# Kernel tuning notes

Hardware: AMD Instinct MI355X
Metric: run time of the kernel (lower is better)

Reference implementation:

```python
import jax, jax.numpy as jnp
import numpy as np

HEADS = 16
D_K = 64
D_MODEL = HEADS * D_K  # 1024
QUERY_DIM = 1024
B, N = 4, 2048


def setup_inputs() -> dict:
    key = jax.random.key(0)
    k1, k2, k3, k4 = jax.random.split(key, 4)
    x = jax.random.normal(k1, (B, N, QUERY_DIM), dtype=jnp.float32)
    # weights stored as [in, out]; torch Linear(in,out,bias=False) is x @ W.T with W [out,in] -- math-equivalent for random init
    Wq = jax.random.normal(k2, (QUERY_DIM, D_MODEL), dtype=jnp.float32) * (QUERY_DIM ** -0.5)
    Wkv = jax.random.normal(k3, (QUERY_DIM, 2 * D_MODEL), dtype=jnp.float32) * (QUERY_DIM ** -0.5)
    Wo = jax.random.normal(k4, (D_MODEL, QUERY_DIM), dtype=jnp.float32) * (D_MODEL ** -0.5)
    return {"x": x, "Wq": Wq, "Wkv": Wkv, "Wo": Wo}


def reference(x, Wq, Wkv, Wo):
    # self-attention: context = x
    scale = D_K ** -0.5
    q = x @ Wq                      # [b, n, h*d]
    kv = x @ Wkv                    # [b, n, 2*h*d]
    k, v = jnp.split(kv, 2, axis=-1)
    # 'b n (h d) -> b h n d'
    def split_heads(t):
        b, n, _ = t.shape
        return t.reshape(b, n, HEADS, D_K).transpose(0, 2, 1, 3)
    q, k, v = map(split_heads, (q, k, v))
    scores = jnp.einsum('bhnd,bhmd->bhnm', q, k) * scale
    attn = jax.nn.softmax(scores, axis=-1)
    out = jnp.einsum('bhnm,bhmd->bhnd', attn, v)
    out = out.transpose(0, 2, 1, 3).reshape(x.shape[0], x.shape[1], D_MODEL)
    return out @ Wo  # dropout is identity at eval
```

## Files before the change

### kernel.cpp

```cpp
#include <hip/hip_runtime.h>
#include <stdint.h>


#define NSEQ   2048
#define BQ     4
#define NTOK   (BQ * NSEQ)
#define DMODEL 1024
#define DK     64
#define HEADS  16

using bf16x8 = __attribute__((ext_vector_type(8))) short;
using u16x8  = __attribute__((ext_vector_type(8))) unsigned short;
using u16x4  = __attribute__((ext_vector_type(4))) unsigned short;
using f32x4  = __attribute__((ext_vector_type(4))) float;

#define AS1C(p) ((const __attribute__((address_space(1))) void*)(p))
#define AS3(p)  ((__attribute__((address_space(3))) void*)(p))

__device__ __forceinline__ unsigned short f2bf(float f) {
    unsigned int u = __float_as_uint(f);
    u += 0x7FFFu + ((u >> 16) & 1u);
    return (unsigned short)(u >> 16);
}


__global__ __launch_bounds__(256) void cvt_x_kernel(const float4* __restrict__ in,
                                                    u16x4* __restrict__ out) {
    int idx = blockIdx.x * 256 + threadIdx.x;
    float4 v = in[idx];
    u16x4 o;
    o[0] = f2bf(v.x); o[1] = f2bf(v.y); o[2] = f2bf(v.z); o[3] = f2bf(v.w);
    out[idx] = o;
}

__global__ __launch_bounds__(256) void transpose_cvt_kernel(const float* __restrict__ in,
                                                            unsigned short* __restrict__ out,
                                                            int K, int Nn) {
    __shared__ float t[32][33];
    int c0 = blockIdx.x * 32;
    int r0 = blockIdx.y * 32;
    int tx = threadIdx.x;
    int ty = threadIdx.y;
#pragma unroll
    for (int i = 0; i < 4; i++) {
        int r = ty + i * 8;
        t[r][tx] = in[(size_t)(r0 + r) * Nn + c0 + tx];
    }
    __syncthreads();
#pragma unroll
    for (int i = 0; i < 4; i++) {
        int r = ty + i * 8;
        out[(size_t)(c0 + r) * K + r0 + tx] = f2bf(t[tx][r]);
    }
}

template <int MODE>
__global__ __launch_bounds__(256) void gemm_bf16_kernel(
    const unsigned short* __restrict__ A,
    const unsigned short* __restrict__ BT,
    unsigned short* __restrict__ C0,
    unsigned short* __restrict__ C1,
    float* __restrict__ CF,
    int M, int N, int K) {
    __shared__ __align__(16) char smem[32768];
    char* As = smem;
    char* Bs = smem + 16384;

    const int tid  = threadIdx.x;
    const int wid  = tid >> 6;
    const int lane = tid & 63;
    const int g    = lane >> 4;
    const int lr   = lane & 15;
    const int wr   = wid >> 1;
    const int wc   = wid & 1;
    const int row0 = blockIdx.y * 128;
    const int col0 = blockIdx.x * 128;

    f32x4 acc[4][4];
#pragma unroll
    for (int i = 0; i < 4; i++)
#pragma unroll
        for (int j = 0; j < 4; j++) acc[i][j] = f32x4{0.f, 0.f, 0.f, 0.f};

    for (int kt = 0; kt < K; kt += 64) {
#pragma unroll
        for (int c = 0; c < 4; c++) {
            int ch  = c * 4 + wid;
            int off = ch * 1024 + lane * 16;
            int row = off >> 7;
            int ss  = ((off >> 4) & 7) ^ (row & 7);
            __builtin_amdgcn_global_load_lds(
                AS1C(A + (size_t)(row0 + row) * K + kt + ss * 8),
                AS3(As + ch * 1024), 16, 0, 0);
        }
#pragma unroll
        for (int c = 0; c < 4; c++) {
            int ch  = c * 4 + wid;
            int off = ch * 1024 + lane * 16;
            int row = off >> 7;
            int ss  = ((off >> 4) & 7) ^ (row & 7);
            __builtin_amdgcn_global_load_lds(
                AS1C(BT + (size_t)(col0 + row) * K + kt + ss * 8),
                AS3(Bs + ch * 1024), 16, 0, 0);
        }
        __syncthreads();

#pragma unroll
        for (int kk = 0; kk < 2; kk++) {
            bf16x8 af[4], bfr[4];
#pragma unroll
            for (int mf = 0; mf < 4; mf++) {
                int row = wr * 64 + mf * 16 + lr;
                int sl  = (kk * 4 + g) ^ (row & 7);
                af[mf]  = *(const bf16x8*)(As + row * 128 + sl * 16);
            }
#pragma unroll
            for (int nf = 0; nf < 4; nf++) {
                int row = wc * 64 + nf * 16 + lr;
                int sl  = (kk * 4 + g) ^ (row & 7);
                bfr[nf] = *(const bf16x8*)(Bs + row * 128 + sl * 16);
            }
#pragma unroll
            for (int mf = 0; mf < 4; mf++)
#pragma unroll
                for (int nf = 0; nf < 4; nf++)
                    acc[mf][nf] = __builtin_amdgcn_mfma_f32_16x16x32_bf16(
                        af[mf], bfr[nf], acc[mf][nf], 0, 0, 0);
        }
        __syncthreads();
    }

    const float SCALE = 0.125f * 1.44269504088896340736f;
#pragma unroll
    for (int mf = 0; mf < 4; mf++)
#pragma unroll
        for (int nf = 0; nf < 4; nf++) {
            if (MODE == 1 && col0 >= 1024) {
                int jj = col0 - 1024 + wc * 64 + nf * 16 + lr;
                int h  = jj >> 6, d = jj & 63;
                int n0 = row0 + wr * 64 + mf * 16 + g * 4;
                int b  = n0 >> 11, nn = n0 & 2047;
                u16x4 pk;
#pragma unroll
                for (int r = 0; r < 4; r++) pk[r] = f2bf(acc[mf][nf][r]);
                *(u16x4*)(C1 + (((size_t)(b * 16 + h)) * 64 + d) * 2048 + nn) = pk;
            } else {
#pragma unroll
                for (int r = 0; r < 4; r++) {
                    int grow = row0 + wr * 64 + mf * 16 + g * 4 + r;
                    int gcol = col0 + wc * 64 + nf * 16 + lr;
                    float v  = acc[mf][nf][r];
                    if (MODE == 2) {
                        CF[(size_t)grow * N + gcol] = v;
                    } else if (MODE == 0) {
                        int b = grow >> 11, n = grow & 2047;
                        int h = gcol >> 6, d = gcol & 63;
                        C0[(((size_t)(b * 16 + h)) * 2048 + n) * 64 + d] = f2bf(v * SCALE);
                    } else {
                        int b = grow >> 11, n = grow & 2047;
                        int h = gcol >> 6, d = gcol & 63;
                        C0[(((size_t)(b * 16 + h)) * 2048 + n) * 64 + d] = f2bf(v);
                    }
                }
            }
        }
}

__global__ __launch_bounds__(256) void attn_fwd_kernel(
    const unsigned short* __restrict__ Q,
    const unsigned short* __restrict__ K,
    const unsigned short* __restrict__ Vt,
    unsigned short* __restrict__ O) {
    __shared__ __align__(16) char smem[32768];

    const int tid  = threadIdx.x;
    const int wid  = tid >> 6;
    const int lane = tid & 63;
    const int g    = lane >> 4;
    const int lr   = lane & 15;
    const int bh   = blockIdx.y;
    const int b    = bh >> 4;
    const int h    = bh & 15;
    const size_t hb = (size_t)bh * NSEQ * DK;
    const unsigned short* Qh  = Q + hb;
    const unsigned short* Kh  = K + hb;
    const unsigned short* Vth = Vt + hb;
    const int qw = blockIdx.x * 64 + wid * 16;

    const int srow  = lane >> 3;
    const int sslot = (lane & 7) ^ srow;
    const int kOff0 = (wid * 8 + srow) * 64 + sslot * 8;
    const int kOff1 = ((wid + 4) * 8 + srow) * 64 + sslot * 8;
    const int vOff0 = (wid * 8 + srow) * 2048 + sslot * 8;
    const int vOff1 = ((wid + 4) * 8 + srow) * 2048 + sslot * 8;

    int kByte[2][4];
#pragma unroll
    for (int kk = 0; kk < 2; kk++)
#pragma unroll
        for (int kb = 0; kb < 4; kb++) {
            int row = (lr >> 2) * 8 + 2 * (lr & 3) + (kb & 1) * 32 + (kb >> 1);
            int sl  = (kk * 4 + g) ^ (row & 7);
            kByte[kk][kb] = row * 128 + sl * 16;
        }
    int vByte[2][4];
#pragma unroll
    for (int kc = 0; kc < 2; kc++)
#pragma unroll
        for (int db = 0; db < 4; db++) {
            int d = db * 16 + lr;
            int sl = (kc * 4 + g) ^ (d & 7);
            vByte[kc][db] = d * 128 + sl * 16;
        }

    bf16x8 qf[2];
#pragma unroll
    for (int kk = 0; kk < 2; kk++)
        qf[kk] = *(const bf16x8*)(Qh + (size_t)(qw + lr) * 64 + kk * 32 + g * 8);

    float l = 0.f;
    f32x4 acc_o[4];
#pragma unroll
    for (int d = 0; d < 4; d++) acc_o[d] = f32x4{0.f, 0.f, 0.f, 0.f};

    auto STAGE = [&](int buf, int kv0) {
        char* Kb = smem + buf * 8192;
        char* Vb = smem + 16384 + buf * 8192;
        __builtin_amdgcn_global_load_lds(AS1C(Kh + (size_t)kv0 * 64 + kOff0),
                                         AS3(Kb + wid * 1024), 16, 0, 0);
        __builtin_amdgcn_global_load_lds(AS1C(Kh + (size_t)kv0 * 64 + kOff1),
                                         AS3(Kb + (wid + 4) * 1024), 16, 0, 0);
        __builtin_amdgcn_global_load_lds(AS1C(Vth + kv0 + vOff0),
                                         AS3(Vb + wid * 1024), 16, 0, 0);
        __builtin_amdgcn_global_load_lds(AS1C(Vth + kv0 + vOff1),
                                         AS3(Vb + (wid + 4) * 1024), 16, 0, 0);
    };

    STAGE(0, 0);
    int cur = 0;

    for (int kvt = 0; kvt < NSEQ / 64; kvt++) {
        __syncthreads();
        if (kvt + 1 < NSEQ / 64) STAGE(cur ^ 1, (kvt + 1) * 64);

        char* Kb = smem + cur * 8192;
        char* Vb = smem + 16384 + cur * 8192;

        f32x4 sc[4];
#pragma unroll
        for (int kb = 0; kb < 4; kb++) sc[kb] = f32x4{0.f, 0.f, 0.f, 0.f};
#pragma unroll
        for (int kk = 0; kk < 2; kk++)
#pragma unroll
            for (int kb = 0; kb < 4; kb++) {
                bf16x8 kf = *(const bf16x8*)(Kb + kByte[kk][kb]);
                sc[kb] = __builtin_amdgcn_mfma_f32_16x16x32_bf16(kf, qf[kk], sc[kb], 0, 0, 0);
            }

        float p[4][4];
#pragma unroll
        for (int kb = 0; kb < 4; kb++)
#pragma unroll
            for (int r = 0; r < 4; r++) {
                float t = sc[kb][r] - 12.0f;
                float e;
                asm("v_exp_f32 %0, %1" : "=v"(e) : "v"(t));
                p[kb][r] = e;
            }
        float s0 = (p[0][0] + p[0][1]) + (p[0][2] + p[0][3]);
        float s1 = (p[1][0] + p[1][1]) + (p[1][2] + p[1][3]);
        float s2 = (p[2][0] + p[2][1]) + (p[2][2] + p[2][3]);
        float s3 = (p[3][0] + p[3][1]) + (p[3][2] + p[3][3]);
        float ls = (s0 + s1) + (s2 + s3);
        ls += __shfl_xor(ls, 16);
        ls += __shfl_xor(ls, 32);
        l += ls;

        bf16x8 pa[2];
#pragma unroll
        for (int kc = 0; kc < 2; kc++) {
            union { unsigned int w[4]; bf16x8 v; } u;
#pragma unroll
            for (int t = 0; t < 4; t++) {
                unsigned int w;
                asm("v_cvt_pk_bf16_f32 %0, %1, %2"
                    : "=v"(w) : "v"(p[kc][t]), "v"(p[kc + 2][t]));
                u.w[t] = w;
            }
            pa[kc] = u.v;
        }

#pragma unroll
        for (int kc = 0; kc < 2; kc++)
#pragma unroll
            for (int db = 0; db < 4; db++) {
                bf16x8 vf = *(const bf16x8*)(Vb + vByte[kc][db]);
                acc_o[db] = __builtin_amdgcn_mfma_f32_16x16x32_bf16(pa[kc], vf, acc_o[db], 0, 0, 0);
            }
        cur ^= 1;
    }

    float linv = 1.f / l;
    float lb[4];
#pragma unroll
    for (int r = 0; r < 4; r++) lb[r] = __shfl(linv, g * 4 + r);
#pragma unroll
    for (int r = 0; r < 4; r++) {
        int n       = qw + g * 4 + r;
        size_t base = ((size_t)(b * NSEQ + n)) * DMODEL + h * 64;
#pragma unroll
        for (int db = 0; db < 4; db++)
            O[base + db * 16 + lr] = f2bf(acc_o[db][r] * lb[r]);
    }
}


extern "C" void kernel_launch(void* const* d_in, const int* in_sizes, int n_in,
                              void* d_out, int out_size, void* d_ws, size_t ws_size,
                              hipStream_t stream) {
    const float* x   = (const float*)d_in[0];
    const float* Wq  = (const float*)d_in[1];
    const float* Wkv = (const float*)d_in[2];
    const float* Wo  = (const float*)d_in[3];
    float* out       = (float*)d_out;

    char* ws = (char*)d_ws;
    unsigned short* xb   = (unsigned short*)(ws);
    unsigned short* WqT  = (unsigned short*)(ws + (16u << 20));
    unsigned short* WkvT = (unsigned short*)(ws + (18u << 20));
    unsigned short* WoT  = (unsigned short*)(ws + (22u << 20));
    unsigned short* Qb   = (unsigned short*)(ws + (24u << 20));
    unsigned short* Kb   = (unsigned short*)(ws + (40u << 20));
    unsigned short* Vbt  = (unsigned short*)(ws + (56u << 20));
    unsigned short* Ob   = xb;
    if (ws_size < (72u << 20)) return;

    cvt_x_kernel<<<8192, 256, 0, stream>>>((const float4*)x, (u16x4*)xb);
    transpose_cvt_kernel<<<dim3(32, 32), dim3(32, 8), 0, stream>>>(Wq, WqT, 1024, 1024);
    transpose_cvt_kernel<<<dim3(64, 32), dim3(32, 8), 0, stream>>>(Wkv, WkvT, 1024, 2048);
    transpose_cvt_kernel<<<dim3(32, 32), dim3(32, 8), 0, stream>>>(Wo, WoT, 1024, 1024);

    gemm_bf16_kernel<0><<<dim3(8, 64), 256, 0, stream>>>(xb, WqT, Qb, nullptr, nullptr,
                                                         NTOK, 1024, 1024);
    gemm_bf16_kernel<1><<<dim3(16, 64), 256, 0, stream>>>(xb, WkvT, Kb, Vbt, nullptr,
                                                          NTOK, 2048, 1024);
    attn_fwd_kernel<<<dim3(32, 64), 256, 0, stream>>>(Qb, Kb, Vbt, Ob);
    gemm_bf16_kernel<2><<<dim3(8, 64), 256, 0, stream>>>(Ob, WoT, nullptr, nullptr, out,
                                                         NTOK, 1024, 1024);
}
```

Measured before the change: 314.8 us.

## Fuse QKV GEMM, double-buffer GEMM LDS, swizzle grids, widen attention tiles

The Q and KV projection weights are written into one concatenated transposed buffer, so a single GEMM launch produces Q, K and transposed V, with the output region picked from the column block. The GEMM now double-buffers its LDS tiles (64KB) so the next K-slice loads while the current one computes, and drops one barrier per iteration. Both GEMM and attention remap block indices with an XCD-style swizzle to improve L2 locality. Each attention wave now handles 32 queries instead of 16, so each K/V fragment read from LDS is reused twice, at the cost of more registers and half as many workgroups.

```diff
diff --git a/kernel.cpp b/kernel.cpp
--- a/kernel.cpp
+++ b/kernel.cpp
@@ -58,13 +58,12 @@
 __global__ __launch_bounds__(256) void gemm_bf16_kernel(
     const unsigned short* __restrict__ A,
     const unsigned short* __restrict__ BT,
-    unsigned short* __restrict__ C0,
-    unsigned short* __restrict__ C1,
+    unsigned short* __restrict__ Cq,
+    unsigned short* __restrict__ Ck,
+    unsigned short* __restrict__ Cv,
     float* __restrict__ CF,
     int M, int N, int K) {
-    __shared__ __align__(16) char smem[32768];
-    char* As = smem;
-    char* Bs = smem + 16384;
+    __shared__ __align__(16) char smem[65536];
 
     const int tid  = threadIdx.x;
     const int wid  = tid >> 6;
@@ -73,38 +72,54 @@
     const int lr   = lane & 15;
     const int wr   = wid >> 1;
     const int wc   = wid & 1;
-    const int row0 = blockIdx.y * 128;
-    const int col0 = blockIdx.x * 128;
-
+
+    const int nwg = gridDim.x * gridDim.y;
+    const int hw  = blockIdx.y * gridDim.x + blockIdx.x;
+    const int swz = (hw & 7) * (nwg >> 3) + (hw >> 3);
+    const int row0 = (swz / gridDim.x) * 128;
+    const int col0 = (swz % gridDim.x) * 128;
+
+    const int ch   = lane >> 2;
+    (void)ch;
     f32x4 acc[4][4];
 #pragma unroll
     for (int i = 0; i < 4; i++)
 #pragma unroll
         for (int j = 0; j < 4; j++) acc[i][j] = f32x4{0.f, 0.f, 0.f, 0.f};
 
-    for (int kt = 0; kt < K; kt += 64) {
+    auto STAGE = [&](int buf, int kt) {
+        char* As = smem + buf * 32768;
+        char* Bs = As + 16384;
 #pragma unroll
         for (int c = 0; c < 4; c++) {
-            int ch  = c * 4 + wid;
-            int off = ch * 1024 + lane * 16;
+            int chk = c * 4 + wid;
+            int off = chk * 1024 + lane * 16;
             int row = off >> 7;
             int ss  = ((off >> 4) & 7) ^ (row & 7);
             __builtin_amdgcn_global_load_lds(
                 AS1C(A + (size_t)(row0 + row) * K + kt + ss * 8),
-                AS3(As + ch * 1024), 16, 0, 0);
+                AS3(As + chk * 1024), 16, 0, 0);
         }
 #pragma unroll
         for (int c = 0; c < 4; c++) {
-            int ch  = c * 4 + wid;
-            int off = ch * 1024 + lane * 16;
+            int chk = c * 4 + wid;
+            int off = chk * 1024 + lane * 16;
             int row = off >> 7;
             int ss  = ((off >> 4) & 7) ^ (row & 7);
             __builtin_amdgcn_global_load_lds(
                 AS1C(BT + (size_t)(col0 + row) * K + kt + ss * 8),
-                AS3(Bs + ch * 1024), 16, 0, 0);
-        }
+                AS3(Bs + chk * 1024), 16, 0, 0);
+        }
+    };
+
+    const int NT = K >> 6;
+    STAGE(0, 0);
+    int cur = 0;
+    for (int kt = 0; kt < NT; kt++) {
         __syncthreads();
-
+        if (kt + 1 < NT) STAGE(cur ^ 1, (kt + 1) * 64);
+        char* As = smem + cur * 32768;
+        char* Bs = As + 16384;
 #pragma unroll
         for (int kk = 0; kk < 2; kk++) {
             bf16x8 af[4], bfr[4];
@@ -127,41 +142,51 @@
                     acc[mf][nf] = __builtin_amdgcn_mfma_f32_16x16x32_bf16(
                         af[mf], bfr[nf], acc[mf][nf], 0, 0, 0);
         }
-        __syncthreads();
+        cur ^= 1;
     }
 
     const float SCALE = 0.125f * 1.44269504088896340736f;
+    const int region = (MODE == 0) ? (col0 >> 10) : 2;
 #pragma unroll
     for (int mf = 0; mf < 4; mf++)
 #pragma unroll
         for (int nf = 0; nf < 4; nf++) {
-            if (MODE == 1 && col0 >= 1024) {
-                int jj = col0 - 1024 + wc * 64 + nf * 16 + lr;
+            if (MODE == 2) {
+#pragma unroll
+                for (int r = 0; r < 4; r++) {
+                    int grow = row0 + wr * 64 + mf * 16 + g * 4 + r;
+                    int gcol = col0 + wc * 64 + nf * 16 + lr;
+                    CF[(size_t)grow * N + gcol] = acc[mf][nf][r];
+                }
+            } else if (region == 0) {
+#pragma unroll
+                for (int r = 0; r < 4; r++) {
+                    int grow = row0 + wr * 64 + mf * 16 + g * 4 + r;
+                    int gcol = col0 + wc * 64 + nf * 16 + lr;
+                    int b = grow >> 11, n = grow & 2047;
+                    int h = gcol >> 6, d = gcol & 63;
+                    Cq[(((size_t)(b * 16 + h)) * 2048 + n) * 64 + d] =
+                        f2bf(acc[mf][nf][r] * SCALE);
+                }
+            } else if (region == 1) {
+#pragma unroll
+                for (int r = 0; r < 4; r++) {
+                    int grow = row0 + wr * 64 + mf * 16 + g * 4 + r;
+                    int jj   = col0 - 1024 + wc * 64 + nf * 16 + lr;
+                    int b = grow >> 11, n = grow & 2047;
+                    int h = jj >> 6, d = jj & 63;
+                    Ck[(((size_t)(b * 16 + h)) * 2048 + n) * 64 + d] =
+                        f2bf(acc[mf][nf][r]);
+                }
+            } else {
+                int jj = col0 - 2048 + wc * 64 + nf * 16 + lr;
                 int h  = jj >> 6, d = jj & 63;
                 int n0 = row0 + wr * 64 + mf * 16 + g * 4;
                 int b  = n0 >> 11, nn = n0 & 2047;
                 u16x4 pk;
 #pragma unroll
                 for (int r = 0; r < 4; r++) pk[r] = f2bf(acc[mf][nf][r]);
-                *(u16x4*)(C1 + (((size_t)(b * 16 + h)) * 64 + d) * 2048 + nn) = pk;
-            } else {
-#pragma unroll
-                for (int r = 0; r < 4; r++) {
-                    int grow = row0 + wr * 64 + mf * 16 + g * 4 + r;
-                    int gcol = col0 + wc * 64 + nf * 16 + lr;
-                    float v  = acc[mf][nf][r];
-                    if (MODE == 2) {
-                        CF[(size_t)grow * N + gcol] = v;
-                    } else if (MODE == 0) {
-                        int b = grow >> 11, n = grow & 2047;
-                        int h = gcol >> 6, d = gcol & 63;
-                        C0[(((size_t)(b * 16 + h)) * 2048 + n) * 64 + d] = f2bf(v * SCALE);
-                    } else {
-                        int b = grow >> 11, n = grow & 2047;
-                        int h = gcol >> 6, d = gcol & 63;
-                        C0[(((size_t)(b * 16 + h)) * 2048 + n) * 64 + d] = f2bf(v);
-                    }
-                }
+                *(u16x4*)(Cv + (((size_t)(b * 16 + h)) * 64 + d) * 2048 + nn) = pk;
             }
         }
 }
@@ -178,14 +203,17 @@
     const int lane = tid & 63;
     const int g    = lane >> 4;
     const int lr   = lane & 15;
-    const int bh   = blockIdx.y;
-    const int b    = bh >> 4;
-    const int h    = bh & 15;
+
+    const int hw  = blockIdx.y * 16 + blockIdx.x;
+    const int swz = (hw & 7) * 128 + (hw >> 3);
+    const int bh  = swz >> 4;
+    const int b   = bh >> 4;
+    const int h   = bh & 15;
     const size_t hb = (size_t)bh * NSEQ * DK;
     const unsigned short* Qh  = Q + hb;
     const unsigned short* Kh  = K + hb;
     const unsigned short* Vth = Vt + hb;
-    const int qw = blockIdx.x * 64 + wid * 16;
+    const int qw = (swz & 15) * 128 + wid * 32;
 
     const int srow  = lane >> 3;
     const int sslot = (lane & 7) ^ srow;
@@ -199,7 +227,7 @@
     for (int kk = 0; kk < 2; kk++)
 #pragma unroll
         for (int kb = 0; kb < 4; kb++) {
-            int row = (lr >> 2) * 8 + 2 * (lr & 3) + (kb & 1) * 32 + (kb >> 1);
+            int row = (lr >> 2) * 8 + (kb >> 1) * 32 + 2 * (lr & 3) + (kb & 1);
             int sl  = (kk * 4 + g) ^ (row & 7);
             kByte[kk][kb] = row * 128 + sl * 16;
         }
@@ -208,20 +236,25 @@
     for (int kc = 0; kc < 2; kc++)
 #pragma unroll
         for (int db = 0; db < 4; db++) {
-            int d = db * 16 + lr;
+            int d  = db * 16 + lr;
             int sl = (kc * 4 + g) ^ (d & 7);
             vByte[kc][db] = d * 128 + sl * 16;
         }
 
-    bf16x8 qf[2];
-#pragma unroll
-    for (int kk = 0; kk < 2; kk++)
-        qf[kk] = *(const bf16x8*)(Qh + (size_t)(qw + lr) * 64 + kk * 32 + g * 8);
-
-    float l = 0.f;
-    f32x4 acc_o[4];
-#pragma unroll
-    for (int d = 0; d < 4; d++) acc_o[d] = f32x4{0.f, 0.f, 0.f, 0.f};
+    bf16x8 qf[2][2];
+#pragma unroll
+    for (int qh = 0; qh < 2; qh++)
+#pragma unroll
+        for (int kk = 0; kk < 2; kk++)
+            qf[qh][kk] = *(const bf16x8*)(Qh + (size_t)(qw + qh * 16 + lr) * 64 +
+                                          kk * 32 + g * 8);
+
+    float lacc[2] = {0.f, 0.f};
+    f32x4 acc_o[2][4];
+#pragma unroll
+    for (int qh = 0; qh < 2; qh++)
+#pragma unroll
+        for (int d = 0; d < 4; d++) acc_o[qh][d] = f32x4{0.f, 0.f, 0.f, 0.f};
 
     auto STAGE = [&](int buf, int kv0) {
         char* Kb = smem + buf * 8192;
@@ -246,48 +279,46 @@
         char* Kb = smem + cur * 8192;
         char* Vb = smem + 16384 + cur * 8192;
 
-        f32x4 sc[4];
-#pragma unroll
-        for (int kb = 0; kb < 4; kb++) sc[kb] = f32x4{0.f, 0.f, 0.f, 0.f};
-#pragma unroll
-        for (int kk = 0; kk < 2; kk++)
-#pragma unroll
-            for (int kb = 0; kb < 4; kb++) {
-                bf16x8 kf = *(const bf16x8*)(Kb + kByte[kk][kb]);
-                sc[kb] = __builtin_amdgcn_mfma_f32_16x16x32_bf16(kf, qf[kk], sc[kb], 0, 0, 0);
-            }
-
-        float p[4][4];
-#pragma unroll
-        for (int kb = 0; kb < 4; kb++)
-#pragma unroll
-            for (int r = 0; r < 4; r++) {
-                float t = sc[kb][r] - 12.0f;
-                float e;
-                asm("v_exp_f32 %0, %1" : "=v"(e) : "v"(t));
-                p[kb][r] = e;
-            }
-        float s0 = (p[0][0] + p[0][1]) + (p[0][2] + p[0][3]);
-        float s1 = (p[1][0] + p[1][1]) + (p[1][2] + p[1][3]);
-        float s2 = (p[2][0] + p[2][1]) + (p[2][2] + p[2][3]);
-        float s3 = (p[3][0] + p[3][1]) + (p[3][2] + p[3][3]);
-        float ls = (s0 + s1) + (s2 + s3);
-        ls += __shfl_xor(ls, 16);
-        ls += __shfl_xor(ls, 32);
-        l += ls;
-
-        bf16x8 pa[2];
+        bf16x8 pa[2][2];
 #pragma unroll
         for (int kc = 0; kc < 2; kc++) {
-            union { unsigned int w[4]; bf16x8 v; } u;
-#pragma unroll
-            for (int t = 0; t < 4; t++) {
-                unsigned int w;
-                asm("v_cvt_pk_bf16_f32 %0, %1, %2"
-                    : "=v"(w) : "v"(p[kc][t]), "v"(p[kc + 2][t]));
-                u.w[t] = w;
-            }
-            pa[kc] = u.v;
+            f32x4 sc[2][2];
+#pragma unroll
+            for (int qh = 0; qh < 2; qh++)
+#pragma unroll
+                for (int kbl = 0; kbl < 2; kbl++) sc[qh][kbl] = f32x4{0.f, 0.f, 0.f, 0.f};
+#pragma unroll
+            for (int kk = 0; kk < 2; kk++)
+#pragma unroll
+                for (int kbl = 0; kbl < 2; kbl++) {
+                    bf16x8 kf = *(const bf16x8*)(Kb + kByte[kk][kc * 2 + kbl]);
+                    sc[0][kbl] = __builtin_amdgcn_mfma_f32_16x16x32_bf16(kf, qf[0][kk], sc[0][kbl], 0, 0, 0);
+                    sc[1][kbl] = __builtin_amdgcn_mfma_f32_16x16x32_bf16(kf, qf[1][kk], sc[1][kbl], 0, 0, 0);
+                }
+#pragma unroll
+            for (int qh = 0; qh < 2; qh++) {
+                float p0[4], p1[4];
+#pragma unroll
+                for (int r = 0; r < 4; r++) {
+                    float t0 = sc[qh][0][r] - 12.0f, e0;
+                    asm("v_exp_f32 %0, %1" : "=v"(e0) : "v"(t0));
+                    p0[r] = e0;
+                    float t1 = sc[qh][1][r] - 12.0f, e1;
+                    asm("v_exp_f32 %0, %1" : "=v"(e1) : "v"(t1));
+                    p1[r] = e1;
+                }
+                lacc[qh] += ((p0[0] + p0[1]) + (p0[2] + p0[3])) +
+                            ((p1[0] + p1[1]) + (p1[2] + p1[3]));
+                union { unsigned int w[4]; bf16x8 v; } u;
+#pragma unroll
+                for (int t = 0; t < 4; t++) {
+                    unsigned int w;
+                    asm("v_cvt_pk_bf16_f32 %0, %1, %2"
+                        : "=v"(w) : "v"(p0[t]), "v"(p1[t]));
+                    u.w[t] = w;
+                }
+                pa[qh][kc] = u.v;
+            }
         }
 
 #pragma unroll
@@ -295,22 +326,29 @@
 #pragma unroll
             for (int db = 0; db < 4; db++) {
                 bf16x8 vf = *(const bf16x8*)(Vb + vByte[kc][db]);
-                acc_o[db] = __builtin_amdgcn_mfma_f32_16x16x32_bf16(pa[kc], vf, acc_o[db], 0, 0, 0);
+                acc_o[0][db] = __builtin_amdgcn_mfma_f32_16x16x32_bf16(pa[0][kc], vf, acc_o[0][db], 0, 0, 0);
+                acc_o[1][db] = __builtin_amdgcn_mfma_f32_16x16x32_bf16(pa[1][kc], vf, acc_o[1][db], 0, 0, 0);
             }
         cur ^= 1;
     }
 
-    float linv = 1.f / l;
-    float lb[4];
-#pragma unroll
-    for (int r = 0; r < 4; r++) lb[r] = __shfl(linv, g * 4 + r);
-#pragma unroll
-    for (int r = 0; r < 4; r++) {
-        int n       = qw + g * 4 + r;
-        size_t base = ((size_t)(b * NSEQ + n)) * DMODEL + h * 64;
-#pragma unroll
-        for (int db = 0; db < 4; db++)
-            O[base + db * 16 + lr] = f2bf(acc_o[db][r] * lb[r]);
+#pragma unroll
+    for (int qh = 0; qh < 2; qh++) {
+        float lv = lacc[qh];
+        lv += __shfl_xor(lv, 16);
+        lv += __shfl_xor(lv, 32);
+        float linv = 1.f / lv;
+        float lb[4];
+#pragma unroll
+        for (int r = 0; r < 4; r++) lb[r] = __shfl(linv, g * 4 + r);
+#pragma unroll
+        for (int r = 0; r < 4; r++) {
+            int n       = qw + qh * 16 + g * 4 + r;
+            size_t base = ((size_t)(b * NSEQ + n)) * DMODEL + h * 64;
+#pragma unroll
+            for (int db = 0; db < 4; db++)
+                O[base + db * 16 + lr] = f2bf(acc_o[qh][db][r] * lb[r]);
+        }
     }
 }
 
@@ -325,26 +363,23 @@
     float* out       = (float*)d_out;
 
     char* ws = (char*)d_ws;
-    unsigned short* xb   = (unsigned short*)(ws);
-    unsigned short* WqT  = (unsigned short*)(ws + (16u << 20));
-    unsigned short* WkvT = (unsigned short*)(ws + (18u << 20));
-    unsigned short* WoT  = (unsigned short*)(ws + (22u << 20));
-    unsigned short* Qb   = (unsigned short*)(ws + (24u << 20));
-    unsigned short* Kb   = (unsigned short*)(ws + (40u << 20));
-    unsigned short* Vbt  = (unsigned short*)(ws + (56u << 20));
-    unsigned short* Ob   = xb;
+    unsigned short* xb     = (unsigned short*)(ws);
+    unsigned short* WqkvT  = (unsigned short*)(ws + (16u << 20));
+    unsigned short* WoT    = (unsigned short*)(ws + (22u << 20));
+    unsigned short* Qb     = (unsigned short*)(ws + (24u << 20));
+    unsigned short* Kb     = (unsigned short*)(ws + (40u << 20));
+    unsigned short* Vbt    = (unsigned short*)(ws + (56u << 20));
+    unsigned short* Ob     = xb;
     if (ws_size < (72u << 20)) return;
 
     cvt_x_kernel<<<8192, 256, 0, stream>>>((const float4*)x, (u16x4*)xb);
-    transpose_cvt_kernel<<<dim3(32, 32), dim3(32, 8), 0, stream>>>(Wq, WqT, 1024, 1024);
-    transpose_cvt_kernel<<<dim3(64, 32), dim3(32, 8), 0, stream>>>(Wkv, WkvT, 1024, 2048);
+    transpose_cvt_kernel<<<dim3(32, 32), dim3(32, 8), 0, stream>>>(Wq, WqkvT, 1024, 1024);
+    transpose_cvt_kernel<<<dim3(64, 32), dim3(32, 8), 0, stream>>>(Wkv, WqkvT + (1024u * 1024u), 1024, 2048);
     transpose_cvt_kernel<<<dim3(32, 32), dim3(32, 8), 0, stream>>>(Wo, WoT, 1024, 1024);
 
-    gemm_bf16_kernel<0><<<dim3(8, 64), 256, 0, stream>>>(xb, WqT, Qb, nullptr, nullptr,
-                                                         NTOK, 1024, 1024);
-    gemm_bf16_kernel<1><<<dim3(16, 64), 256, 0, stream>>>(xb, WkvT, Kb, Vbt, nullptr,
-                                                          NTOK, 2048, 1024);
-    attn_fwd_kernel<<<dim3(32, 64), 256, 0, stream>>>(Qb, Kb, Vbt, Ob);
-    gemm_bf16_kernel<2><<<dim3(8, 64), 256, 0, stream>>>(Ob, WoT, nullptr, nullptr, out,
-                                                         NTOK, 1024, 1024);
-}
+    gemm_bf16_kernel<0><<<dim3(24, 64), 256, 0, stream>>>(xb, WqkvT, Qb, Kb, Vbt,
+                                                          nullptr, NTOK, 3072, 1024);
+    attn_fwd_kernel<<<dim3(16, 64), 256, 0, stream>>>(Qb, Kb, Vbt, Ob);
+    gemm_bf16_kernel<2><<<dim3(8, 64), 256, 0, stream>>>(Ob, WoT, nullptr, nullptr, nullptr,
+                                                         out, NTOK, 1024, 1024);
+}
```

After: 271.8 us. 1.16x faster.
